# Kernel optimization log

Measured on AMD Instinct MI355X. Metric: run time of the kernel, lower is better.

Reference implementation:

```python
import jax, jax.numpy as jnp
import numpy as np

NUM_EXPERTS = 64
TOP_K = 2
B, S, EMB, MLP = 4, 2048, 1024, 2048


def setup_inputs() -> dict:
    key = jax.random.key(0)
    k1, k2, k3, k4, k5 = jax.random.split(key, 5)
    inputs = jax.random.normal(k1, (B, S, EMB), dtype=jnp.float32)
    gate_kernel = jax.random.normal(k2, (EMB, NUM_EXPERTS), dtype=jnp.float32) / np.sqrt(EMB)
    w0 = jax.random.normal(k3, (NUM_EXPERTS, EMB, MLP), dtype=jnp.float32) / np.sqrt(EMB)
    w1 = jax.random.normal(k4, (NUM_EXPERTS, EMB, MLP), dtype=jnp.float32) / np.sqrt(EMB)
    wo = jax.random.normal(k5, (NUM_EXPERTS, MLP, EMB), dtype=jnp.float32) / np.sqrt(MLP)
    return {"inputs": inputs, "gate_kernel": gate_kernel, "w0": w0, "w1": w1, "wo": wo}


def reference(inputs, gate_kernel, w0, w1, wo):
    b, s, e = inputs.shape
    x = inputs.reshape(b * s, e)                                  # [T, E]
    # Router (DenseGeneral gate)
    gate_logits = jnp.einsum('te,ex->tx', x, gate_kernel)         # [T, X]
    # permute(): top-k gating + sort tokens by expert
    weights, selected = jax.lax.top_k(gate_logits, TOP_K)         # [T, K]
    weights = jax.nn.softmax(weights.astype(jnp.float32), axis=-1)
    flat_experts = selected.reshape(-1)                           # [T*K]
    sort_idx = jnp.argsort(flat_experts)                          # [T*K]
    token_idx = sort_idx // TOP_K
    sorted_x = jnp.take(x, token_idx, axis=0)                     # [T*K, E]
    group_sizes = jnp.bincount(flat_experts, length=NUM_EXPERTS).astype(jnp.int32)
    # grouped GEMMs (gated FFN: silu(x@w0) * (x@w1) @ wo)
    h0 = jax.lax.ragged_dot(sorted_x, w0, group_sizes)            # [T*K, M]
    h1 = jax.lax.ragged_dot(sorted_x, w1, group_sizes)            # [T*K, M]
    inter = jax.nn.silu(h0) * h1
    out_sorted = jax.lax.ragged_dot(inter, wo, group_sizes)       # [T*K, E]
    # unpermute(): restore token order, weighted combine over top-k
    unsorted = jnp.take(out_sorted, jnp.argsort(sort_idx), axis=0)
    per_tok = unsorted.reshape(b * s, TOP_K, e)
    out = jnp.einsum('BKE,BK->BE', per_tok.astype(jnp.float32), weights)
    return out.reshape(b, s, e)
```

## Files before the change

kernel.cpp:

```cpp
#include <hip/hip_runtime.h>
#include <hip/hip_bf16.h>
#include <math.h>

#define NTOK   8192
#define NEXP   64
#define EMBD   1024
#define MLPD   2048
#define TOPK   2
#define NFLAT  (NTOK * TOPK)
#define BKD    32
#define BPAD   40
#define MAXCH  8

typedef __attribute__((ext_vector_type(4))) float  f32x4;
typedef __attribute__((ext_vector_type(2))) float  f32x2;
typedef __attribute__((ext_vector_type(8))) __bf16 bf16x8;

#define OFF_COUNTS 0
#define OFF_BASE   256
#define OFF_RUN    512
#define OFF_EFLAT  1024
#define OFF_WFLAT  (1024 + 65536)
#define OFF_ROWTOK (1024 + 2 * 65536)
#define OFF_F2R    (1024 + 3 * 65536)
#define OFF_INTER  (1024 + 4 * 65536)
#define OFF_OS     (OFF_INTER + (size_t)NFLAT * MLPD * 2)
#define NEED_F32   (OFF_OS + (size_t)NFLAT * EMBD * 4)

__global__ __launch_bounds__(256) void router_topk(
    const float* __restrict__ x, const float* __restrict__ gk,
    int* __restrict__ e_flat, float* __restrict__ w_flat) {
  int t = blockIdx.x * 4 + (threadIdx.x >> 6);
  int l = threadIdx.x & 63;
  const float* xr = x + (size_t)t * EMBD;
  float acc = 0.f;
  #pragma unroll 8
  for (int i = 0; i < EMBD; ++i)
    acc = fmaf(xr[i], gk[i * NEXP + l], acc);
  float m = acc;
  for (int o = 32; o; o >>= 1) m = fmaxf(m, __shfl_xor(m, o));
  unsigned long long b1 = __ballot(acc == m);
  int i1 = __ffsll(b1) - 1;
  float v2 = (l == i1) ? -INFINITY : acc;
  float m2 = v2;
  for (int o = 32; o; o >>= 1) m2 = fmaxf(m2, __shfl_xor(m2, o));
  unsigned long long b2 = __ballot(v2 == m2);
  int i2 = __ffsll(b2) - 1;
  if (l == 0) {
    float e2 = expf(m2 - m);
    float inv = 1.f / (1.f + e2);
    e_flat[2 * t] = i1;  e_flat[2 * t + 1] = i2;
    w_flat[2 * t] = inv; w_flat[2 * t + 1] = e2 * inv;
  }
}

__global__ void hist_k(const int* __restrict__ ef, int* __restrict__ counts) {
  int j = blockIdx.x * 256 + threadIdx.x;
  if (j < NFLAT) atomicAdd(&counts[ef[j]], 1);
}

__global__ void scan_k(const int* __restrict__ counts, int* __restrict__ base) {
  if (threadIdx.x == 0) {
    int s = 0;
    for (int e = 0; e < NEXP; ++e) { base[e] = s; s += counts[e]; }
  }
}

__global__ void scatter_k(const int* __restrict__ ef, const int* __restrict__ base,
                          int* __restrict__ run, int* __restrict__ rowtok,
                          int* __restrict__ f2r) {
  int j = blockIdx.x * 256 + threadIdx.x;
  if (j < NFLAT) {
    int e = ef[j];
    int r = base[e] + atomicAdd(&run[e], 1);
    f2r[j] = r;
    rowtok[r] = j >> 1;
  }
}

__global__ __launch_bounds__(256, 2) void gemm1_k(
    const float* __restrict__ x, const float* __restrict__ w0,
    const float* __restrict__ w1, const int* __restrict__ counts,
    const int* __restrict__ base, const int* __restrict__ rowtok,
    __hip_bfloat16* __restrict__ inter) {
  int e = blockIdx.z;
  int Me = counts[e];
  int mc = blockIdx.y;
  if (mc * 128 >= Me) return;
  int rs = base[e];
  int nb = blockIdx.x * 128;
  int t = threadIdx.x;
  int wv = t >> 6, l = t & 63;
  int wr = wv >> 1, wc = wv & 1;
  int lg = l >> 4, li = l & 15;

  __shared__ __bf16 Ash[2][128 * BKD];
  __shared__ __bf16 B0sh[2][128 * BPAD];
  __shared__ __bf16 B1sh[2][128 * BPAD];

  int ra = t >> 1, kh = t & 1;
  int rga = mc * 128 + ra; rga = rga < Me ? rga : Me - 1;
  const float* asrc = x + (size_t)rowtok[rs + rga] * EMBD + kh * 16;
  int n2 = t & 63, kg = t >> 6;
  const size_t weoff = (size_t)e * EMBD * MLPD;
  const float* b0src = w0 + weoff + (size_t)(kg * 8) * MLPD + nb + n2 * 2;
  const float* b1src = w1 + weoff + (size_t)(kg * 8) * MLPD + nb + n2 * 2;

  f32x4 va[4];
  f32x2 vb0[8], vb1[8];

  auto LOAD = [&](int kk) {
    #pragma unroll
    for (int j = 0; j < 4; ++j)
      va[j] = *(const f32x4*)(asrc + kk + j * 4);
    #pragma unroll
    for (int q = 0; q < 8; ++q) {
      vb0[q] = *(const f32x2*)(b0src + (size_t)(kk + q) * MLPD);
      vb1[q] = *(const f32x2*)(b1src + (size_t)(kk + q) * MLPD);
    }
  };
  auto CVTW = [&](int c) {
    bf16x8 a0, a1;
    #pragma unroll
    for (int i = 0; i < 4; ++i) {
      a0[i] = (__bf16)va[0][i]; a0[4 + i] = (__bf16)va[1][i];
      a1[i] = (__bf16)va[2][i]; a1[4 + i] = (__bf16)va[3][i];
    }
    *(bf16x8*)(&Ash[c][ra * BKD + kh * 16])     = a0;
    *(bf16x8*)(&Ash[c][ra * BKD + kh * 16 + 8]) = a1;
    bf16x8 c0, c1, d0, d1;
    #pragma unroll
    for (int q = 0; q < 8; ++q) {
      c0[q] = (__bf16)vb0[q][0]; c1[q] = (__bf16)vb0[q][1];
      d0[q] = (__bf16)vb1[q][0]; d1[q] = (__bf16)vb1[q][1];
    }
    *(bf16x8*)(&B0sh[c][(n2 * 2)     * BPAD + kg * 8]) = c0;
    *(bf16x8*)(&B0sh[c][(n2 * 2 + 1) * BPAD + kg * 8]) = c1;
    *(bf16x8*)(&B1sh[c][(n2 * 2)     * BPAD + kg * 8]) = d0;
    *(bf16x8*)(&B1sh[c][(n2 * 2 + 1) * BPAD + kg * 8]) = d1;
  };

  f32x4 acc0[4][4], acc1[4][4];
  #pragma unroll
  for (int i = 0; i < 4; ++i)
    #pragma unroll
    for (int j = 0; j < 4; ++j) {
      acc0[i][j] = (f32x4){0.f, 0.f, 0.f, 0.f};
      acc1[i][j] = (f32x4){0.f, 0.f, 0.f, 0.f};
    }

  LOAD(0);
  CVTW(0);
  int c = 0;
  const int NT = EMBD / BKD;
  for (int ks = 0; ks < NT; ++ks) {
    __syncthreads();
    if (ks + 1 < NT) LOAD((ks + 1) * BKD);
    bf16x8 af[4], bf0[4], bf1[4];
    #pragma unroll
    for (int mf = 0; mf < 4; ++mf)
      af[mf] = *(const bf16x8*)(&Ash[c][(wr * 64 + mf * 16 + li) * BKD + lg * 8]);
    #pragma unroll
    for (int nf = 0; nf < 4; ++nf) {
      bf0[nf] = *(const bf16x8*)(&B0sh[c][(wc * 64 + nf * 16 + li) * BPAD + lg * 8]);
      bf1[nf] = *(const bf16x8*)(&B1sh[c][(wc * 64 + nf * 16 + li) * BPAD + lg * 8]);
    }
    #pragma unroll
    for (int nf = 0; nf < 4; ++nf)
      #pragma unroll
      for (int mf = 0; mf < 4; ++mf) {
        acc0[mf][nf] = __builtin_amdgcn_mfma_f32_16x16x32_bf16(af[mf], bf0[nf], acc0[mf][nf], 0, 0, 0);
        acc1[mf][nf] = __builtin_amdgcn_mfma_f32_16x16x32_bf16(af[mf], bf1[nf], acc1[mf][nf], 0, 0, 0);
      }
    if (ks + 1 < NT) { CVTW(c ^ 1); c ^= 1; }
  }

  #pragma unroll
  for (int mf = 0; mf < 4; ++mf)
    #pragma unroll
    for (int i = 0; i < 4; ++i) {
      int rl = mc * 128 + wr * 64 + mf * 16 + lg * 4 + i;
      if (rl < Me) {
        size_t rowoff = (size_t)(rs + rl) * MLPD;
        #pragma unroll
        for (int nf = 0; nf < 4; ++nf) {
          float h0 = acc0[mf][nf][i], h1 = acc1[mf][nf][i];
          float s = h0 / (1.f + expf(-h0)) * h1;
          inter[rowoff + nb + wc * 64 + nf * 16 + li] = (__hip_bfloat16)s;
        }
      }
    }
}

template <typename OS_T>
__global__ __launch_bounds__(256, 2) void gemm2_k(
    const __hip_bfloat16* __restrict__ inter, const float* __restrict__ wo,
    const int* __restrict__ counts, const int* __restrict__ base,
    OS_T* __restrict__ os) {
  int e = blockIdx.z;
  int Me = counts[e];
  int mc = blockIdx.y;
  if (mc * 128 >= Me) return;
  int rs = base[e];
  int nb = blockIdx.x * 128;
  int t = threadIdx.x;
  int wv = t >> 6, l = t & 63;
  int wr = wv >> 1, wc = wv & 1;
  int lg = l >> 4, li = l & 15;

  __shared__ __bf16 Ash[2][128 * BKD];
  __shared__ __bf16 Bsh[2][128 * BPAD];

  int ra = t >> 1, kh = t & 1;
  int rga = mc * 128 + ra; rga = rga < Me ? rga : Me - 1;
  const __hip_bfloat16* asrc = inter + (size_t)(rs + rga) * MLPD + kh * 16;
  int n2 = t & 63, kg = t >> 6;
  const size_t weoff = (size_t)e * MLPD * EMBD;
  const float* bsrc = wo + weoff + (size_t)(kg * 8) * EMBD + nb + n2 * 2;

  bf16x8 va[2];
  f32x2 vb[8];

  auto LOAD = [&](int kk) {
    va[0] = *(const bf16x8*)(asrc + kk);
    va[1] = *(const bf16x8*)(asrc + kk + 8);
    #pragma unroll
    for (int q = 0; q < 8; ++q)
      vb[q] = *(const f32x2*)(bsrc + (size_t)(kk + q) * EMBD);
  };
  auto CVTW = [&](int c) {
    *(bf16x8*)(&Ash[c][ra * BKD + kh * 16])     = va[0];
    *(bf16x8*)(&Ash[c][ra * BKD + kh * 16 + 8]) = va[1];
    bf16x8 c0, c1;
    #pragma unroll
    for (int q = 0; q < 8; ++q) {
      c0[q] = (__bf16)vb[q][0]; c1[q] = (__bf16)vb[q][1];
    }
    *(bf16x8*)(&Bsh[c][(n2 * 2)     * BPAD + kg * 8]) = c0;
    *(bf16x8*)(&Bsh[c][(n2 * 2 + 1) * BPAD + kg * 8]) = c1;
  };

  f32x4 acc[4][4];
  #pragma unroll
  for (int i = 0; i < 4; ++i)
    #pragma unroll
    for (int j = 0; j < 4; ++j) acc[i][j] = (f32x4){0.f, 0.f, 0.f, 0.f};

  LOAD(0);
  CVTW(0);
  int c = 0;
  const int NT = MLPD / BKD;
  for (int ks = 0; ks < NT; ++ks) {
    __syncthreads();
    if (ks + 1 < NT) LOAD((ks + 1) * BKD);
    bf16x8 af[4], bfr[4];
    #pragma unroll
    for (int mf = 0; mf < 4; ++mf)
      af[mf] = *(const bf16x8*)(&Ash[c][(wr * 64 + mf * 16 + li) * BKD + lg * 8]);
    #pragma unroll
    for (int nf = 0; nf < 4; ++nf)
      bfr[nf] = *(const bf16x8*)(&Bsh[c][(wc * 64 + nf * 16 + li) * BPAD + lg * 8]);
    #pragma unroll
    for (int nf = 0; nf < 4; ++nf)
      #pragma unroll
      for (int mf = 0; mf < 4; ++mf)
        acc[mf][nf] = __builtin_amdgcn_mfma_f32_16x16x32_bf16(af[mf], bfr[nf], acc[mf][nf], 0, 0, 0);
    if (ks + 1 < NT) { CVTW(c ^ 1); c ^= 1; }
  }

  #pragma unroll
  for (int mf = 0; mf < 4; ++mf)
    #pragma unroll
    for (int i = 0; i < 4; ++i) {
      int rl = mc * 128 + wr * 64 + mf * 16 + lg * 4 + i;
      if (rl < Me) {
        size_t rowoff = (size_t)(rs + rl) * EMBD;
        #pragma unroll
        for (int nf = 0; nf < 4; ++nf)
          os[rowoff + nb + wc * 64 + nf * 16 + li] = (OS_T)acc[mf][nf][i];
      }
    }
}

template <typename OS_T>
__global__ __launch_bounds__(256) void combine_k(
    const OS_T* __restrict__ os, const int* __restrict__ f2r,
    const float* __restrict__ wf, float* __restrict__ out) {
  int t = blockIdx.x;
  int c = threadIdx.x * 4;
  int r0 = f2r[2 * t], r1 = f2r[2 * t + 1];
  float wa = wf[2 * t], wb = wf[2 * t + 1];
  const OS_T* pa = os + (size_t)r0 * EMBD + c;
  const OS_T* pb = os + (size_t)r1 * EMBD + c;
  float4 o;
  o.x = wa * (float)pa[0] + wb * (float)pb[0];
  o.y = wa * (float)pa[1] + wb * (float)pb[1];
  o.z = wa * (float)pa[2] + wb * (float)pb[2];
  o.w = wa * (float)pa[3] + wb * (float)pb[3];
  *(float4*)(out + (size_t)t * EMBD + c) = o;
}

extern "C" void kernel_launch(void* const* d_in, const int* in_sizes, int n_in,
                              void* d_out, int out_size, void* d_ws, size_t ws_size,
                              hipStream_t stream) {
  const float* x  = (const float*)d_in[0];
  const float* gk = (const float*)d_in[1];
  const float* w0 = (const float*)d_in[2];
  const float* w1 = (const float*)d_in[3];
  const float* wo = (const float*)d_in[4];
  float* out = (float*)d_out;
  char* ws = (char*)d_ws;

  int*   counts = (int*)(ws + OFF_COUNTS);
  int*   basep  = (int*)(ws + OFF_BASE);
  int*   run    = (int*)(ws + OFF_RUN);
  int*   ef     = (int*)(ws + OFF_EFLAT);
  float* wfl    = (float*)(ws + OFF_WFLAT);
  int*   rowtok = (int*)(ws + OFF_ROWTOK);
  int*   f2r    = (int*)(ws + OFF_F2R);
  __hip_bfloat16* inter = (__hip_bfloat16*)(ws + OFF_INTER);

  hipMemsetAsync(ws, 0, 1024, stream);
  router_topk<<<NTOK / 4, 256, 0, stream>>>(x, gk, ef, wfl);
  hist_k<<<NFLAT / 256, 256, 0, stream>>>(ef, counts);
  scan_k<<<1, 64, 0, stream>>>(counts, basep);
  scatter_k<<<NFLAT / 256, 256, 0, stream>>>(ef, basep, run, rowtok, f2r);
  gemm1_k<<<dim3(16, MAXCH, 64), 256, 0, stream>>>(x, w0, w1, counts, basep, rowtok, inter);

  if (ws_size >= NEED_F32) {
    float* os = (float*)(ws + OFF_OS);
    gemm2_k<float><<<dim3(8, MAXCH, 64), 256, 0, stream>>>(inter, wo, counts, basep, os);
    combine_k<float><<<NTOK, 256, 0, stream>>>(os, f2r, wfl, out);
  } else {
    __hip_bfloat16* os = (__hip_bfloat16*)(ws + OFF_OS);
    gemm2_k<__hip_bfloat16><<<dim3(8, MAXCH, 64), 256, 0, stream>>>(inter, wo, counts, basep, os);
    combine_k<__hip_bfloat16><<<NTOK, 256, 0, stream>>>(os, f2r, wfl, out);
  }
}
```

Baseline: 1.156 ms.

## Shrink grouped-GEMM N tiles to 64 and loop over row chunks inside each block

Both grouped GEMMs now use 64-wide N tiles, and one block per (N tile, expert) walks every 128-row chunk of that expert. Previously the grid was fixed at MAXCH=8 chunks and most blocks exited early. The change also removes the silent cap of 1024 rows per expert, pads the A shared tile, and raises the launch-bounds occupancy targets. The cost is serialized row chunks inside a block when experts are imbalanced, and lower MFMA reuse per loaded tile.

```diff
diff --git a/kernel.cpp b/kernel.cpp
--- a/kernel.cpp
+++ b/kernel.cpp
@@ -9,12 +9,13 @@
 #define TOPK   2
 #define NFLAT  (NTOK * TOPK)
 #define BKD    32
+#define APAD   40
 #define BPAD   40
-#define MAXCH  8
 
 typedef __attribute__((ext_vector_type(4))) float  f32x4;
 typedef __attribute__((ext_vector_type(2))) float  f32x2;
 typedef __attribute__((ext_vector_type(8))) __bf16 bf16x8;
+typedef __attribute__((ext_vector_type(4))) __bf16 bf16x4;
 
 #define OFF_COUNTS 0
 #define OFF_BASE   256
@@ -78,208 +79,202 @@
   }
 }
 
-__global__ __launch_bounds__(256, 2) void gemm1_k(
+__global__ __launch_bounds__(256, 3) void gemm1_k(
     const float* __restrict__ x, const float* __restrict__ w0,
     const float* __restrict__ w1, const int* __restrict__ counts,
     const int* __restrict__ base, const int* __restrict__ rowtok,
     __hip_bfloat16* __restrict__ inter) {
-  int e = blockIdx.z;
+  int e = blockIdx.y;
   int Me = counts[e];
-  int mc = blockIdx.y;
-  if (mc * 128 >= Me) return;
+  if (Me == 0) return;
   int rs = base[e];
-  int nb = blockIdx.x * 128;
+  int nb = blockIdx.x * 64;
   int t = threadIdx.x;
   int wv = t >> 6, l = t & 63;
   int wr = wv >> 1, wc = wv & 1;
   int lg = l >> 4, li = l & 15;
 
-  __shared__ __bf16 Ash[2][128 * BKD];
-  __shared__ __bf16 B0sh[2][128 * BPAD];
-  __shared__ __bf16 B1sh[2][128 * BPAD];
+  __shared__ __bf16 Ash[2][128 * APAD];
+  __shared__ __bf16 Bsh[2][2][64 * BPAD];
 
   int ra = t >> 1, kh = t & 1;
-  int rga = mc * 128 + ra; rga = rga < Me ? rga : Me - 1;
-  const float* asrc = x + (size_t)rowtok[rs + rga] * EMBD + kh * 16;
-  int n2 = t & 63, kg = t >> 6;
-  const size_t weoff = (size_t)e * EMBD * MLPD;
-  const float* b0src = w0 + weoff + (size_t)(kg * 8) * MLPD + nb + n2 * 2;
-  const float* b1src = w1 + weoff + (size_t)(kg * 8) * MLPD + nb + n2 * 2;
+  int mat = t >> 7;
+  int n2 = (t >> 2) & 31, kq = t & 3;
+  const float* wsrc = (mat ? w1 : w0) + (size_t)e * EMBD * MLPD + nb + n2 * 2;
 
   f32x4 va[4];
-  f32x2 vb0[8], vb1[8];
-
-  auto LOAD = [&](int kk) {
+  f32x2 vb[8];
+
+  for (int mc = 0; mc * 128 < Me; ++mc) {
+    int rga = mc * 128 + ra; rga = rga < Me ? rga : Me - 1;
+    const float* asrc = x + (size_t)rowtok[rs + rga] * EMBD + kh * 16;
+
+    auto LOAD = [&](int kk) {
+      #pragma unroll
+      for (int j = 0; j < 4; ++j) va[j] = *(const f32x4*)(asrc + kk + j * 4);
+      #pragma unroll
+      for (int q = 0; q < 8; ++q)
+        vb[q] = *(const f32x2*)(wsrc + (size_t)(kk + kq * 8 + q) * MLPD);
+    };
+    auto CVTW = [&](int c) {
+      bf16x8 a0, a1;
+      #pragma unroll
+      for (int i = 0; i < 4; ++i) {
+        a0[i] = (__bf16)va[0][i]; a0[4 + i] = (__bf16)va[1][i];
+        a1[i] = (__bf16)va[2][i]; a1[4 + i] = (__bf16)va[3][i];
+      }
+      *(bf16x8*)(&Ash[c][ra * APAD + kh * 16])     = a0;
+      *(bf16x8*)(&Ash[c][ra * APAD + kh * 16 + 8]) = a1;
+      bf16x8 c0, c1;
+      #pragma unroll
+      for (int q = 0; q < 8; ++q) { c0[q] = (__bf16)vb[q][0]; c1[q] = (__bf16)vb[q][1]; }
+      *(bf16x8*)(&Bsh[c][mat][(n2 * 2)     * BPAD + kq * 8]) = c0;
+      *(bf16x8*)(&Bsh[c][mat][(n2 * 2 + 1) * BPAD + kq * 8]) = c1;
+    };
+
+    f32x4 acc0[4][2], acc1[4][2];
     #pragma unroll
-    for (int j = 0; j < 4; ++j)
-      va[j] = *(const f32x4*)(asrc + kk + j * 4);
-    #pragma unroll
-    for (int q = 0; q < 8; ++q) {
-      vb0[q] = *(const f32x2*)(b0src + (size_t)(kk + q) * MLPD);
-      vb1[q] = *(const f32x2*)(b1src + (size_t)(kk + q) * MLPD);
+    for (int i = 0; i < 4; ++i)
+      #pragma unroll
+      for (int j = 0; j < 2; ++j) {
+        acc0[i][j] = (f32x4){0.f, 0.f, 0.f, 0.f};
+        acc1[i][j] = (f32x4){0.f, 0.f, 0.f, 0.f};
+      }
+
+    LOAD(0);
+    __syncthreads();
+    CVTW(0);
+    int cb = 0;
+    const int NT = EMBD / BKD;
+    for (int ks = 0; ks < NT; ++ks) {
+      __syncthreads();
+      if (ks + 1 < NT) LOAD((ks + 1) * BKD);
+      bf16x8 af[4], bf0[2], bf1[2];
+      #pragma unroll
+      for (int mf = 0; mf < 4; ++mf)
+        af[mf] = *(const bf16x8*)(&Ash[cb][(wr * 64 + mf * 16 + li) * APAD + lg * 8]);
+      #pragma unroll
+      for (int nf = 0; nf < 2; ++nf) {
+        bf0[nf] = *(const bf16x8*)(&Bsh[cb][0][(wc * 32 + nf * 16 + li) * BPAD + lg * 8]);
+        bf1[nf] = *(const bf16x8*)(&Bsh[cb][1][(wc * 32 + nf * 16 + li) * BPAD + lg * 8]);
+      }
+      #pragma unroll
+      for (int nf = 0; nf < 2; ++nf)
+        #pragma unroll
+        for (int mf = 0; mf < 4; ++mf) {
+          acc0[mf][nf] = __builtin_amdgcn_mfma_f32_16x16x32_bf16(af[mf], bf0[nf], acc0[mf][nf], 0, 0, 0);
+          acc1[mf][nf] = __builtin_amdgcn_mfma_f32_16x16x32_bf16(af[mf], bf1[nf], acc1[mf][nf], 0, 0, 0);
+        }
+      if (ks + 1 < NT) { CVTW(cb ^ 1); cb ^= 1; }
     }
-  };
-  auto CVTW = [&](int c) {
-    bf16x8 a0, a1;
-    #pragma unroll
-    for (int i = 0; i < 4; ++i) {
-      a0[i] = (__bf16)va[0][i]; a0[4 + i] = (__bf16)va[1][i];
-      a1[i] = (__bf16)va[2][i]; a1[4 + i] = (__bf16)va[3][i];
-    }
-    *(bf16x8*)(&Ash[c][ra * BKD + kh * 16])     = a0;
-    *(bf16x8*)(&Ash[c][ra * BKD + kh * 16 + 8]) = a1;
-    bf16x8 c0, c1, d0, d1;
-    #pragma unroll
-    for (int q = 0; q < 8; ++q) {
-      c0[q] = (__bf16)vb0[q][0]; c1[q] = (__bf16)vb0[q][1];
-      d0[q] = (__bf16)vb1[q][0]; d1[q] = (__bf16)vb1[q][1];
-    }
-    *(bf16x8*)(&B0sh[c][(n2 * 2)     * BPAD + kg * 8]) = c0;
-    *(bf16x8*)(&B0sh[c][(n2 * 2 + 1) * BPAD + kg * 8]) = c1;
-    *(bf16x8*)(&B1sh[c][(n2 * 2)     * BPAD + kg * 8]) = d0;
-    *(bf16x8*)(&B1sh[c][(n2 * 2 + 1) * BPAD + kg * 8]) = d1;
-  };
-
-  f32x4 acc0[4][4], acc1[4][4];
-  #pragma unroll
-  for (int i = 0; i < 4; ++i)
-    #pragma unroll
-    for (int j = 0; j < 4; ++j) {
-      acc0[i][j] = (f32x4){0.f, 0.f, 0.f, 0.f};
-      acc1[i][j] = (f32x4){0.f, 0.f, 0.f, 0.f};
-    }
-
-  LOAD(0);
-  CVTW(0);
-  int c = 0;
-  const int NT = EMBD / BKD;
-  for (int ks = 0; ks < NT; ++ks) {
-    __syncthreads();
-    if (ks + 1 < NT) LOAD((ks + 1) * BKD);
-    bf16x8 af[4], bf0[4], bf1[4];
+
     #pragma unroll
     for (int mf = 0; mf < 4; ++mf)
-      af[mf] = *(const bf16x8*)(&Ash[c][(wr * 64 + mf * 16 + li) * BKD + lg * 8]);
-    #pragma unroll
-    for (int nf = 0; nf < 4; ++nf) {
-      bf0[nf] = *(const bf16x8*)(&B0sh[c][(wc * 64 + nf * 16 + li) * BPAD + lg * 8]);
-      bf1[nf] = *(const bf16x8*)(&B1sh[c][(wc * 64 + nf * 16 + li) * BPAD + lg * 8]);
-    }
-    #pragma unroll
-    for (int nf = 0; nf < 4; ++nf)
-      #pragma unroll
-      for (int mf = 0; mf < 4; ++mf) {
-        acc0[mf][nf] = __builtin_amdgcn_mfma_f32_16x16x32_bf16(af[mf], bf0[nf], acc0[mf][nf], 0, 0, 0);
-        acc1[mf][nf] = __builtin_amdgcn_mfma_f32_16x16x32_bf16(af[mf], bf1[nf], acc1[mf][nf], 0, 0, 0);
-      }
-    if (ks + 1 < NT) { CVTW(c ^ 1); c ^= 1; }
-  }
-
-  #pragma unroll
-  for (int mf = 0; mf < 4; ++mf)
-    #pragma unroll
-    for (int i = 0; i < 4; ++i) {
-      int rl = mc * 128 + wr * 64 + mf * 16 + lg * 4 + i;
-      if (rl < Me) {
-        size_t rowoff = (size_t)(rs + rl) * MLPD;
-        #pragma unroll
-        for (int nf = 0; nf < 4; ++nf) {
-          float h0 = acc0[mf][nf][i], h1 = acc1[mf][nf][i];
-          float s = h0 / (1.f + expf(-h0)) * h1;
-          inter[rowoff + nb + wc * 64 + nf * 16 + li] = (__hip_bfloat16)s;
+      #pragma unroll
+      for (int i = 0; i < 4; ++i) {
+        int rl = mc * 128 + wr * 64 + mf * 16 + lg * 4 + i;
+        if (rl < Me) {
+          size_t rowoff = (size_t)(rs + rl) * MLPD;
+          #pragma unroll
+          for (int nf = 0; nf < 2; ++nf) {
+            float h0 = acc0[mf][nf][i], h1 = acc1[mf][nf][i];
+            float s = h0 / (1.f + expf(-h0)) * h1;
+            inter[rowoff + nb + wc * 32 + nf * 16 + li] = (__hip_bfloat16)s;
+          }
         }
       }
-    }
+  }
 }
 
 template <typename OS_T>
-__global__ __launch_bounds__(256, 2) void gemm2_k(
+__global__ __launch_bounds__(256, 4) void gemm2_k(
     const __hip_bfloat16* __restrict__ inter, const float* __restrict__ wo,
     const int* __restrict__ counts, const int* __restrict__ base,
     OS_T* __restrict__ os) {
-  int e = blockIdx.z;
+  int e = blockIdx.y;
   int Me = counts[e];
-  int mc = blockIdx.y;
-  if (mc * 128 >= Me) return;
+  if (Me == 0) return;
   int rs = base[e];
-  int nb = blockIdx.x * 128;
+  int nb = blockIdx.x * 64;
   int t = threadIdx.x;
   int wv = t >> 6, l = t & 63;
   int wr = wv >> 1, wc = wv & 1;
   int lg = l >> 4, li = l & 15;
 
-  __shared__ __bf16 Ash[2][128 * BKD];
-  __shared__ __bf16 Bsh[2][128 * BPAD];
+  __shared__ __bf16 Ash[2][128 * APAD];
+  __shared__ __bf16 Bsh[2][64 * BPAD];
 
   int ra = t >> 1, kh = t & 1;
-  int rga = mc * 128 + ra; rga = rga < Me ? rga : Me - 1;
-  const __hip_bfloat16* asrc = inter + (size_t)(rs + rga) * MLPD + kh * 16;
-  int n2 = t & 63, kg = t >> 6;
+  int n2 = (t >> 3) & 31, kqq = t & 7;
   const size_t weoff = (size_t)e * MLPD * EMBD;
-  const float* bsrc = wo + weoff + (size_t)(kg * 8) * EMBD + nb + n2 * 2;
+  const float* bsrc = wo + weoff + nb + n2 * 2;
 
   bf16x8 va[2];
-  f32x2 vb[8];
-
-  auto LOAD = [&](int kk) {
-    va[0] = *(const bf16x8*)(asrc + kk);
-    va[1] = *(const bf16x8*)(asrc + kk + 8);
+  f32x2 vb[4];
+
+  for (int mc = 0; mc * 128 < Me; ++mc) {
+    int rga = mc * 128 + ra; rga = rga < Me ? rga : Me - 1;
+    const __hip_bfloat16* asrc = inter + (size_t)(rs + rga) * MLPD + kh * 16;
+
+    auto LOAD = [&](int kk) {
+      va[0] = *(const bf16x8*)(asrc + kk);
+      va[1] = *(const bf16x8*)(asrc + kk + 8);
+      #pragma unroll
+      for (int q = 0; q < 4; ++q)
+        vb[q] = *(const f32x2*)(bsrc + (size_t)(kk + kqq * 4 + q) * EMBD);
+    };
+    auto CVTW = [&](int c) {
+      *(bf16x8*)(&Ash[c][ra * APAD + kh * 16])     = va[0];
+      *(bf16x8*)(&Ash[c][ra * APAD + kh * 16 + 8]) = va[1];
+      bf16x4 c0, c1;
+      #pragma unroll
+      for (int q = 0; q < 4; ++q) { c0[q] = (__bf16)vb[q][0]; c1[q] = (__bf16)vb[q][1]; }
+      *(bf16x4*)(&Bsh[c][(n2 * 2)     * BPAD + kqq * 4]) = c0;
+      *(bf16x4*)(&Bsh[c][(n2 * 2 + 1) * BPAD + kqq * 4]) = c1;
+    };
+
+    f32x4 acc[4][2];
     #pragma unroll
-    for (int q = 0; q < 8; ++q)
-      vb[q] = *(const f32x2*)(bsrc + (size_t)(kk + q) * EMBD);
-  };
-  auto CVTW = [&](int c) {
-    *(bf16x8*)(&Ash[c][ra * BKD + kh * 16])     = va[0];
-    *(bf16x8*)(&Ash[c][ra * BKD + kh * 16 + 8]) = va[1];
-    bf16x8 c0, c1;
-    #pragma unroll
-    for (int q = 0; q < 8; ++q) {
-      c0[q] = (__bf16)vb[q][0]; c1[q] = (__bf16)vb[q][1];
+    for (int i = 0; i < 4; ++i)
+      #pragma unroll
+      for (int j = 0; j < 2; ++j) acc[i][j] = (f32x4){0.f, 0.f, 0.f, 0.f};
+
+    LOAD(0);
+    __syncthreads();
+    CVTW(0);
+    int cb = 0;
+    const int NT = MLPD / BKD;
+    for (int ks = 0; ks < NT; ++ks) {
+      __syncthreads();
+      if (ks + 1 < NT) LOAD((ks + 1) * BKD);
+      bf16x8 af[4], bfr[2];
+      #pragma unroll
+      for (int mf = 0; mf < 4; ++mf)
+        af[mf] = *(const bf16x8*)(&Ash[cb][(wr * 64 + mf * 16 + li) * APAD + lg * 8]);
+      #pragma unroll
+      for (int nf = 0; nf < 2; ++nf)
+        bfr[nf] = *(const bf16x8*)(&Bsh[cb][(wc * 32 + nf * 16 + li) * BPAD + lg * 8]);
+      #pragma unroll
+      for (int nf = 0; nf < 2; ++nf)
+        #pragma unroll
+        for (int mf = 0; mf < 4; ++mf)
+          acc[mf][nf] = __builtin_amdgcn_mfma_f32_16x16x32_bf16(af[mf], bfr[nf], acc[mf][nf], 0, 0, 0);
+      if (ks + 1 < NT) { CVTW(cb ^ 1); cb ^= 1; }
     }
-    *(bf16x8*)(&Bsh[c][(n2 * 2)     * BPAD + kg * 8]) = c0;
-    *(bf16x8*)(&Bsh[c][(n2 * 2 + 1) * BPAD + kg * 8]) = c1;
-  };
-
-  f32x4 acc[4][4];
-  #pragma unroll
-  for (int i = 0; i < 4; ++i)
-    #pragma unroll
-    for (int j = 0; j < 4; ++j) acc[i][j] = (f32x4){0.f, 0.f, 0.f, 0.f};
-
-  LOAD(0);
-  CVTW(0);
-  int c = 0;
-  const int NT = MLPD / BKD;
-  for (int ks = 0; ks < NT; ++ks) {
-    __syncthreads();
-    if (ks + 1 < NT) LOAD((ks + 1) * BKD);
-    bf16x8 af[4], bfr[4];
+
     #pragma unroll
     for (int mf = 0; mf < 4; ++mf)
-      af[mf] = *(const bf16x8*)(&Ash[c][(wr * 64 + mf * 16 + li) * BKD + lg * 8]);
-    #pragma unroll
-    for (int nf = 0; nf < 4; ++nf)
-      bfr[nf] = *(const bf16x8*)(&Bsh[c][(wc * 64 + nf * 16 + li) * BPAD + lg * 8]);
-    #pragma unroll
-    for (int nf = 0; nf < 4; ++nf)
-      #pragma unroll
-      for (int mf = 0; mf < 4; ++mf)
-        acc[mf][nf] = __builtin_amdgcn_mfma_f32_16x16x32_bf16(af[mf], bfr[nf], acc[mf][nf], 0, 0, 0);
-    if (ks + 1 < NT) { CVTW(c ^ 1); c ^= 1; }
-  }
-
-  #pragma unroll
-  for (int mf = 0; mf < 4; ++mf)
-    #pragma unroll
-    for (int i = 0; i < 4; ++i) {
-      int rl = mc * 128 + wr * 64 + mf * 16 + lg * 4 + i;
-      if (rl < Me) {
-        size_t rowoff = (size_t)(rs + rl) * EMBD;
-        #pragma unroll
-        for (int nf = 0; nf < 4; ++nf)
-          os[rowoff + nb + wc * 64 + nf * 16 + li] = (OS_T)acc[mf][nf][i];
-      }
-    }
+      #pragma unroll
+      for (int i = 0; i < 4; ++i) {
+        int rl = mc * 128 + wr * 64 + mf * 16 + lg * 4 + i;
+        if (rl < Me) {
+          size_t rowoff = (size_t)(rs + rl) * EMBD;
+          #pragma unroll
+          for (int nf = 0; nf < 2; ++nf)
+            os[rowoff + nb + wc * 32 + nf * 16 + li] = (OS_T)acc[mf][nf][i];
+        }
+      }
+  }
 }
 
 template <typename OS_T>
@@ -325,15 +320,15 @@
   hist_k<<<NFLAT / 256, 256, 0, stream>>>(ef, counts);
   scan_k<<<1, 64, 0, stream>>>(counts, basep);
   scatter_k<<<NFLAT / 256, 256, 0, stream>>>(ef, basep, run, rowtok, f2r);
-  gemm1_k<<<dim3(16, MAXCH, 64), 256, 0, stream>>>(x, w0, w1, counts, basep, rowtok, inter);
+  gemm1_k<<<dim3(MLPD / 64, NEXP), 256, 0, stream>>>(x, w0, w1, counts, basep, rowtok, inter);
 
   if (ws_size >= NEED_F32) {
     float* os = (float*)(ws + OFF_OS);
-    gemm2_k<float><<<dim3(8, MAXCH, 64), 256, 0, stream>>>(inter, wo, counts, basep, os);
+    gemm2_k<float><<<dim3(EMBD / 64, NEXP), 256, 0, stream>>>(inter, wo, counts, basep, os);
     combine_k<float><<<NTOK, 256, 0, stream>>>(os, f2r, wfl, out);
   } else {
     __hip_bfloat16* os = (__hip_bfloat16*)(ws + OFF_OS);
-    gemm2_k<__hip_bfloat16><<<dim3(8, MAXCH, 64), 256, 0, stream>>>(inter, wo, counts, basep, os);
+    gemm2_k<__hip_bfloat16><<<dim3(EMBD / 64, NEXP), 256, 0, stream>>>(inter, wo, counts, basep, os);
     combine_k<__hip_bfloat16><<<NTOK, 256, 0, stream>>>(os, f2r, wfl, out);
   }
 }
```

Measured after the change: 1.618 ms. +39.9%, slower.
